# Performance work log

Hardware: AMD Instinct MI355X
Metric: run time of the kernel (lower is better)

Reference implementation:

```python
import jax, jax.numpy as jnp
import numpy as np

N = 96
M = 96
# visual field constants
L_V_EX, S_V_EX, L_V_IN, S_V_IN = 1.6, 3.5, 1.23, 6.3
FV, TAU_V, UPS_V, P_V, K_V = 1.0, 3.0, 3.0, 0.3, 7.0
# auditory field constants
L_A_EX, S_A_EX, L_A_IN, S_A_IN = 1.0, 5.3, 0.8, 11.8
FA, TAU_A, UPS_A, P_A, K_A = 1.0, 3.0, 3.0, 0.3, 3.0
# multisensory field constants
L_M_EX, S_M_EX, L_M_IN, S_M_IN = 3.8, 3.5, 3.3, 6.2
TAU_M, UPS_M, P_M = 3.0, 3.0, 0.3


def _torus_sqdist():
    # squared toroidal distance components: dx2[i,h], dy2[j,k]
    ii = jnp.arange(N, dtype=jnp.float32)
    jj = jnp.arange(M, dtype=jnp.float32)
    dx = jnp.abs(ii[:, None] - ii[None, :])
    dx = jnp.minimum(dx, N - dx)
    dy = jnp.abs(jj[:, None] - jj[None, :])
    dy = jnp.minimum(dy, M - dy)
    # aux[i,j,h,k] = dx[i,h]^2 + dy[j,k]^2
    return dx[:, None, :, None] ** 2 + dy[None, :, None, :] ** 2


def _dog(aux, l_ex, s_ex, l_in, s_in):
    # Faithful to source: exp(-aux/2 * sigma**2) == exp(-0.5*aux*sigma^2)
    return l_ex * jnp.exp(-0.5 * aux * (s_ex ** 2)) - l_in * jnp.exp(-0.5 * aux * (s_in ** 2))


def setup_inputs() -> dict:
    key = jax.random.key(0)
    ks = jax.random.split(key, 7)
    return {
        "video": jax.random.normal(ks[0], (32, 1024), dtype=jnp.float32),
        "audio": jax.random.normal(ks[1], (32, 2048), dtype=jnp.float32),
        "rf_v": jax.random.normal(ks[2], (N, M, 1024), dtype=jnp.float32) * (1.0 / np.sqrt(1024.0)),
        "rf_a": jax.random.normal(ks[3], (N, M, 2048), dtype=jnp.float32) * (1.0 / np.sqrt(2048.0)),
        "na_v": jax.random.normal(ks[4], (N, M), dtype=jnp.float32),
        "na_a": jax.random.normal(ks[5], (N, M), dtype=jnp.float32),
        "na_m": jax.random.normal(ks[6], (N, M), dtype=jnp.float32),
    }


def reference(video, audio, rf_v, rf_a, na_v, na_a, na_m):
    aux = _torus_sqdist()  # (N, M, N, M)
    syn_v = _dog(aux, L_V_EX, S_V_EX, L_V_IN, S_V_IN)
    syn_a = _dog(aux, L_A_EX, S_A_EX, L_A_IN, S_A_IN)
    syn_m = _dog(aux, L_M_EX, S_M_EX, L_M_IN, S_M_IN)

    # external inputs: sum over feature dim -> (B, N, M)
    ext_v = jnp.einsum('bv,ijv->bij', video, rf_v)
    ext_a = jnp.einsum('ba,ija->bij', audio, rf_a)

    # all-pairs neighbor inputs: neighbor[i,j] = sum_{h,k} act[h,k] * syn[i,j,h,k]
    nb_v = jnp.einsum('ijhk,hk->ij', syn_v, na_v)
    nb_a = jnp.einsum('ijhk,hk->ij', syn_a, na_a)

    coll_v = FV * na_m
    coll_a = FA * na_m

    na_v_new = na_v * (TAU_V - 1.0) / TAU_V + (1.0 / TAU_V) * jax.nn.sigmoid(
        (ext_v + nb_v - UPS_V + coll_v) * P_V)  # (B, N, M)
    na_a_new = na_a * (TAU_A - 1.0) / TAU_A + (1.0 / TAU_A) * jax.nn.sigmoid(
        (ext_a + nb_a - UPS_A + coll_a) * P_A)  # (B, N, M)

    nb_m = jnp.einsum('ijhk,hk->ij', syn_m, na_m)
    na_m_new = na_m * (TAU_M - 1.0) / TAU_M + (1.0 / TAU_M) * jax.nn.sigmoid(
        (K_V * na_v_new + K_A * na_a_new + nb_m - UPS_M) * P_M)  # (B, N, M)
    return na_m_new
```

## Files before the change

### kernel.cpp

```cpp
#include <hip/hip_runtime.h>
#include <math.h>

#define NN   96
#define NPOS (96*96)
#define BB   32
#define KV   1024
#define KA   2048
#define KCH  512
#define NCHV (KV/KCH)
#define NCHA (KA/KCH)
#define PT16 (NPOS/16)
#define NBLK_V (NCHV*PT16)
#define NBLK_A (NCHA*PT16)

#define PARTV_OFF 0
#define PARTA_OFF (NCHV*BB*NPOS)
#define CPT_OFF   (PARTA_OFF + NCHA*BB*NPOS)
#define AFV_OFF   (CPT_OFF + 6*NPOS)
#define AFV_SLOTS ((KV/32)*2*64)
#define AFA_OFF   (AFV_OFF + AFV_SLOTS*4)
#define AFA_SLOTS ((KA/32)*2*64)

typedef __bf16 bf16x8 __attribute__((ext_vector_type(8)));
typedef float  f32x4  __attribute__((ext_vector_type(4)));

__global__ __launch_bounds__(256) void nbT_kernel(
    const float* __restrict__ na_v, const float* __restrict__ na_a,
    const float* __restrict__ na_m, const float* __restrict__ video,
    const float* __restrict__ audio, float* __restrict__ ws)
{
    __shared__ float G[96][100];
    __shared__ float act_s[96][100];
    __shared__ float T1t[24][100];

    if (blockIdx.x >= 24) {
        const int e = (blockIdx.x - 24) * 256 + threadIdx.x;
        const float* src; bf16x8* dst; int K, el;
        if (e < AFV_SLOTS) { src = video; K = KV; dst = (bf16x8*)(ws + AFV_OFF); el = e; }
        else               { src = audio; K = KA; dst = (bf16x8*)(ws + AFA_OFF); el = e - AFV_SLOTS; }
        const int l  = el & 63;
        const int hb = (el >> 6) & 1;
        const int sg = el >> 7;
        const int b  = hb * 16 + (l & 15);
        const int k0 = sg * 32 + ((l >> 4) << 3);
        const float4 f0 = *(const float4*)&src[(size_t)b * K + k0];
        const float4 f1 = *(const float4*)&src[(size_t)b * K + k0 + 4];
        bf16x8 v;
        v[0] = (__bf16)f0.x; v[1] = (__bf16)f0.y; v[2] = (__bf16)f0.z; v[3] = (__bf16)f0.w;
        v[4] = (__bf16)f1.x; v[5] = (__bf16)f1.y; v[6] = (__bf16)f1.z; v[7] = (__bf16)f1.w;
        dst[el] = v;
        return;
    }

    const int c  = blockIdx.x >> 2;
    const int js = (blockIdx.x & 3) * 24;
    float l, s;
    if      (c == 0) { l =  1.60f; s = 3.5f;  }
    else if (c == 1) { l = -1.23f; s = 6.3f;  }
    else if (c == 2) { l =  1.00f; s = 5.3f;  }
    else if (c == 3) { l = -0.80f; s = 11.8f; }
    else if (c == 4) { l =  3.80f; s = 3.5f;  }
    else             { l = -3.30f; s = 6.2f;  }
    const float s2 = s * s;
    const int f = c >> 1;
    const float* act = (f == 0) ? na_v : (f == 1) ? na_a : na_m;
    const int tid = threadIdx.x;
    float* cpt = ws + CPT_OFF;

    for (int idx = tid; idx < 9216; idx += 256) {
        int j = idx / 96, k = idx - j * 96;
        int d = abs(j - k); d = min(d, 96 - d);
        G[j][k]     = __expf(-0.5f * (float)(d * d) * s2);
        act_s[j][k] = act[idx];
    }
    __syncthreads();

    const int hg3 = (tid >> 3) * 3;
    const int jl3 = (tid & 7) * 3;

    float t1[3][3] = {};
    for (int k0 = 0; k0 < 96; k0 += 4) {
        float4 av[3], gv[3];
        #pragma unroll
        for (int r = 0; r < 3; r++) {
            av[r] = *(const float4*)&act_s[hg3 + r][k0];
            gv[r] = *(const float4*)&G[js + jl3 + r][k0];
        }
        #pragma unroll
        for (int hh = 0; hh < 3; hh++)
            #pragma unroll
            for (int jj = 0; jj < 3; jj++)
                t1[hh][jj] += av[hh].x * gv[jj].x + av[hh].y * gv[jj].y
                            + av[hh].z * gv[jj].z + av[hh].w * gv[jj].w;
    }
    #pragma unroll
    for (int hh = 0; hh < 3; hh++)
        #pragma unroll
        for (int jj = 0; jj < 3; jj++)
            T1t[jl3 + jj][hg3 + hh] = t1[hh][jj];
    __syncthreads();

    float o[3][3] = {};
    for (int h0 = 0; h0 < 96; h0 += 4) {
        float4 gv[3], tv[3];
        #pragma unroll
        for (int r = 0; r < 3; r++) {
            gv[r] = *(const float4*)&G[hg3 + r][h0];
            tv[r] = *(const float4*)&T1t[jl3 + r][h0];
        }
        #pragma unroll
        for (int ii = 0; ii < 3; ii++)
            #pragma unroll
            for (int jj = 0; jj < 3; jj++)
                o[ii][jj] += gv[ii].x * tv[jj].x + gv[ii].y * tv[jj].y
                           + gv[ii].z * tv[jj].z + gv[ii].w * tv[jj].w;
    }
    #pragma unroll
    for (int ii = 0; ii < 3; ii++)
        #pragma unroll
        for (int jj = 0; jj < 3; jj++)
            cpt[c * NPOS + (hg3 + ii) * 96 + (js + jl3 + jj)] = l * o[ii][jj];
}

__global__ __launch_bounds__(64) void ext_mfma(
    const float* __restrict__ rf_v, const float* __restrict__ rf_a,
    float* __restrict__ ws)
{
    const int bid = blockIdx.x;
    const float* rf; const bf16x8* af; float* part; int K;
    int chunk, pt;
    if (bid < NBLK_V) {
        chunk = bid / PT16; pt = bid - chunk * PT16;
        rf = rf_v; K = KV;
        af = (const bf16x8*)(ws + AFV_OFF);
        part = ws + PARTV_OFF + (size_t)chunk * (BB * NPOS);
    } else {
        const int idx = bid - NBLK_V;
        chunk = idx / PT16; pt = idx - chunk * PT16;
        rf = rf_a; K = KA;
        af = (const bf16x8*)(ws + AFA_OFF);
        part = ws + PARTA_OFF + (size_t)chunk * (BB * NPOS);
    }
    const int kbase = chunk * KCH;
    const int l  = threadIdx.x;
    const int p0 = pt * 16;
    const int prow = p0 + (l & 15);
    const int koff = (l >> 4) * 8;
    const float4* bp = (const float4*)(rf + (size_t)prow * K + kbase + koff);
    const bf16x8* ap = af + (kbase >> 5) * 128 + l;

    f32x4 acc0 = {0.f, 0.f, 0.f, 0.f};
    f32x4 acc1 = {0.f, 0.f, 0.f, 0.f};

    #pragma unroll 4
    for (int st = 0; st < KCH / 32; ++st) {
        bf16x8 a0 = ap[st * 128];
        bf16x8 a1 = ap[st * 128 + 64];
        float4 f0 = bp[st * 8];
        float4 f1 = bp[st * 8 + 1];
        bf16x8 bv;
        bv[0] = (__bf16)f0.x; bv[1] = (__bf16)f0.y; bv[2] = (__bf16)f0.z; bv[3] = (__bf16)f0.w;
        bv[4] = (__bf16)f1.x; bv[5] = (__bf16)f1.y; bv[6] = (__bf16)f1.z; bv[7] = (__bf16)f1.w;
        acc0 = __builtin_amdgcn_mfma_f32_16x16x32_bf16(a0, bv, acc0, 0, 0, 0);
        acc1 = __builtin_amdgcn_mfma_f32_16x16x32_bf16(a1, bv, acc1, 0, 0, 0);
    }

    const int pcol  = p0 + (l & 15);
    const int brow0 = (l >> 4) * 4;
    #pragma unroll
    for (int r = 0; r < 4; ++r) {
        part[(size_t)(brow0 + r) * NPOS + pcol]        = acc0[r];
        part[(size_t)(16 + brow0 + r) * NPOS + pcol]   = acc1[r];
    }
}

__global__ __launch_bounds__(256) void combine_kernel(
    const float* __restrict__ na_v, const float* __restrict__ na_a,
    const float* __restrict__ na_m, const float* __restrict__ ws,
    float* __restrict__ out)
{
    const int npq = NPOS >> 2;
    const int t = blockIdx.x * 256 + threadIdx.x;
    if (t >= BB * npq) return;
    const int b  = t / npq;
    const int p0 = (t - b * npq) << 2;

    float4 ev = {0.f, 0.f, 0.f, 0.f}, ea = {0.f, 0.f, 0.f, 0.f};
    #pragma unroll
    for (int c = 0; c < NCHV; c++) {
        float4 x = *(const float4*)&ws[PARTV_OFF + (size_t)c * (BB * NPOS) + (size_t)b * NPOS + p0];
        ev.x += x.x; ev.y += x.y; ev.z += x.z; ev.w += x.w;
    }
    #pragma unroll
    for (int c = 0; c < NCHA; c++) {
        float4 x = *(const float4*)&ws[PARTA_OFF + (size_t)c * (BB * NPOS) + (size_t)b * NPOS + p0];
        ea.x += x.x; ea.y += x.y; ea.z += x.z; ea.w += x.w;
    }
    const float* cpt = ws + CPT_OFF;
    float4 q0 = *(const float4*)&cpt[0 * NPOS + p0];
    float4 q1 = *(const float4*)&cpt[1 * NPOS + p0];
    float4 q2 = *(const float4*)&cpt[2 * NPOS + p0];
    float4 q3 = *(const float4*)&cpt[3 * NPOS + p0];
    float4 q4 = *(const float4*)&cpt[4 * NPOS + p0];
    float4 q5 = *(const float4*)&cpt[5 * NPOS + p0];
    float4 nv = *(const float4*)&na_v[p0];
    float4 na = *(const float4*)&na_a[p0];
    float4 nm = *(const float4*)&na_m[p0];

    float evs[4] = {ev.x, ev.y, ev.z, ev.w};
    float eas[4] = {ea.x, ea.y, ea.z, ea.w};
    float nbv[4] = {q0.x + q1.x, q0.y + q1.y, q0.z + q1.z, q0.w + q1.w};
    float nba[4] = {q2.x + q3.x, q2.y + q3.y, q2.z + q3.z, q2.w + q3.w};
    float nbm[4] = {q4.x + q5.x, q4.y + q5.y, q4.z + q5.z, q4.w + q5.w};
    float nvs[4] = {nv.x, nv.y, nv.z, nv.w};
    float nas[4] = {na.x, na.y, na.z, na.w};
    float nms[4] = {nm.x, nm.y, nm.z, nm.w};

    float4 o;
    float* os = (float*)&o;
    #pragma unroll
    for (int u = 0; u < 4; u++) {
        const float xv = (evs[u] + nbv[u] - 3.0f + nms[u]) * 0.3f;
        const float nav_new = nvs[u] * (2.f / 3.f) + (1.f / 3.f) / (1.f + __expf(-xv));
        const float xa = (eas[u] + nba[u] - 3.0f + nms[u]) * 0.3f;
        const float naa_new = nas[u] * (2.f / 3.f) + (1.f / 3.f) / (1.f + __expf(-xa));
        const float xm = (7.0f * nav_new + 3.0f * naa_new + nbm[u] - 3.0f) * 0.3f;
        os[u] = nms[u] * (2.f / 3.f) + (1.f / 3.f) / (1.f + __expf(-xm));
    }
    *(float4*)&out[(size_t)b * NPOS + p0] = o;
}

extern "C" void kernel_launch(void* const* d_in, const int* in_sizes, int n_in,
                              void* d_out, int out_size, void* d_ws, size_t ws_size,
                              hipStream_t stream) {
    const float* video = (const float*)d_in[0];
    const float* audio = (const float*)d_in[1];
    const float* rf_v  = (const float*)d_in[2];
    const float* rf_a  = (const float*)d_in[3];
    const float* na_v  = (const float*)d_in[4];
    const float* na_a  = (const float*)d_in[5];
    const float* na_m  = (const float*)d_in[6];
    float* ws  = (float*)d_ws;
    float* out = (float*)d_out;

    nbT_kernel<<<72, 256, 0, stream>>>(na_v, na_a, na_m, video, audio, ws);
    ext_mfma<<<NBLK_V + NBLK_A, 64, 0, stream>>>(rf_v, rf_a, ws);
    combine_kernel<<<(BB * NPOS / 4 + 255) / 256, 256, 0, stream>>>(
        na_v, na_a, na_m, ws, out);
}
```

Before: 41.31 us.

## Pipeline ext GEMM through LDS with async global_load_lds and larger K chunks

Reworks the external-input MFMA kernel so each wave streams rf and activation tiles into a 4-deep LDS ring buffer via global_load_lds, using an XOR swizzle and explicit vmcnt waits. Global loads are overlapped with MFMA compute. The K chunk also grows from 512 to 1024, which cuts the partial-sum buffers (video is now one chunk, audio two) and shrinks the reduction in the combine kernel. The cost is fewer, longer blocks, which lowers parallelism, and a fragile pipeline built on hand-written inline asm.

```diff
diff --git a/kernel.cpp b/kernel.cpp
--- a/kernel.cpp
+++ b/kernel.cpp
@@ -6,16 +6,13 @@
 #define BB   32
 #define KV   1024
 #define KA   2048
-#define KCH  512
-#define NCHV (KV/KCH)
-#define NCHA (KA/KCH)
-#define PT16 (NPOS/16)
-#define NBLK_V (NCHV*PT16)
-#define NBLK_A (NCHA*PT16)
-
-#define PARTV_OFF 0
-#define PARTA_OFF (NCHV*BB*NPOS)
-#define CPT_OFF   (PARTA_OFF + NCHA*BB*NPOS)
+
+#define JOBS_A (2*576)
+
+#define EXTV_OFF  0
+#define EXTA0_OFF (BB*NPOS)
+#define EXTA1_OFF (2*BB*NPOS)
+#define CPT_OFF   (3*BB*NPOS)
 #define AFV_OFF   (CPT_OFF + 6*NPOS)
 #define AFV_SLOTS ((KV/32)*2*64)
 #define AFA_OFF   (AFV_OFF + AFV_SLOTS*4)
@@ -23,6 +20,9 @@
 
 typedef __bf16 bf16x8 __attribute__((ext_vector_type(8)));
 typedef float  f32x4  __attribute__((ext_vector_type(4)));
+typedef const __attribute__((address_space(1))) void* gas1_t;
+typedef __attribute__((address_space(3))) void*       las3_t;
+typedef const __attribute__((address_space(3))) char* lds3c_t;
 
 __global__ __launch_bounds__(256) void nbT_kernel(
     const float* __restrict__ na_v, const float* __restrict__ na_a,
@@ -126,51 +126,97 @@
     const float* __restrict__ rf_v, const float* __restrict__ rf_a,
     float* __restrict__ ws)
 {
+    __shared__ char lds[16384];
+    char* ldsc = (char*)lds;
     const int bid = blockIdx.x;
-    const float* rf; const bf16x8* af; float* part; int K;
-    int chunk, pt;
-    if (bid < NBLK_V) {
-        chunk = bid / PT16; pt = bid - chunk * PT16;
-        rf = rf_v; K = KV;
-        af = (const bf16x8*)(ws + AFV_OFF);
-        part = ws + PARTV_OFF + (size_t)chunk * (BB * NPOS);
+    const int l   = threadIdx.x;
+
+    const float* rf; const bf16x8* af; float* ext; int K, kb, pt;
+    if (bid < JOBS_A) {
+        const int c = bid / 576; pt = bid - c * 576;
+        rf = rf_a; K = KA; kb = c << 10;
+        af  = (const bf16x8*)(ws + AFA_OFF);
+        ext = ws + EXTA0_OFF + c * (BB * NPOS);
     } else {
-        const int idx = bid - NBLK_V;
-        chunk = idx / PT16; pt = idx - chunk * PT16;
-        rf = rf_a; K = KA;
-        af = (const bf16x8*)(ws + AFA_OFF);
-        part = ws + PARTA_OFF + (size_t)chunk * (BB * NPOS);
-    }
-    const int kbase = chunk * KCH;
-    const int l  = threadIdx.x;
-    const int p0 = pt * 16;
-    const int prow = p0 + (l & 15);
-    const int koff = (l >> 4) * 8;
-    const float4* bp = (const float4*)(rf + (size_t)prow * K + kbase + koff);
-    const bf16x8* ap = af + (kbase >> 5) * 128 + l;
+        pt = bid - JOBS_A; rf = rf_v; K = KV; kb = 0;
+        af  = (const bf16x8*)(ws + AFV_OFF);
+        ext = ws + EXTV_OFF;
+    }
+    const int p0 = pt << 4;
+
+    const int r8   = l >> 3;
+    const int csrc = (l & 7) ^ (r8 & 7);
+    const float*  rf0 = rf + (size_t)(p0 + r8) * K + kb + csrc * 4;
+    const float*  rf1 = rf0 + (size_t)8 * K;
+    const bf16x8* afA = af + (kb >> 5) * 128 + l;
+    const bf16x8* afB = afA + 64;
+
+    const int row   = l & 15, g = l >> 4;
+    const int roffA = row * 128 + ((((g << 1)    ) ^ (row & 7)) << 4);
+    const int roffB = row * 128 + ((((g << 1) | 1) ^ (row & 7)) << 4);
+    const int aoff  = l * 16;
+
+#define STAGE(tt, dd)                                                          \
+    do {                                                                       \
+        const int t_ = (tt);                                                   \
+        __builtin_amdgcn_global_load_lds((gas1_t)(rf0 + t_ * 32),              \
+            (las3_t)(ldsc + (dd) * 4096), 16, 0, 0);                           \
+        __builtin_amdgcn_global_load_lds((gas1_t)(rf1 + t_ * 32),              \
+            (las3_t)(ldsc + (dd) * 4096 + 1024), 16, 0, 0);                    \
+        __builtin_amdgcn_global_load_lds((gas1_t)(afA + t_ * 128),             \
+            (las3_t)(ldsc + (dd) * 4096 + 2048), 16, 0, 0);                    \
+        __builtin_amdgcn_global_load_lds((gas1_t)(afB + t_ * 128),             \
+            (las3_t)(ldsc + (dd) * 4096 + 3072), 16, 0, 0);                    \
+    } while (0)
+
+#define ITER(tt, dd, WAIT, DO_STAGE)                                           \
+    {                                                                          \
+        asm volatile("s_waitcnt vmcnt(" #WAIT ")");                            \
+        f32x4 rA, rB; bf16x8 av0, av1;                                         \
+        asm volatile("ds_read_b128 %0, %1" : "=v"(rA)                          \
+                     : "v"((lds3c_t)(ldsc + (dd) * 4096 + roffA)));            \
+        asm volatile("ds_read_b128 %0, %1" : "=v"(rB)                          \
+                     : "v"((lds3c_t)(ldsc + (dd) * 4096 + roffB)));            \
+        asm volatile("ds_read_b128 %0, %1" : "=v"(av0)                         \
+                     : "v"((lds3c_t)(ldsc + (dd) * 4096 + 2048 + aoff)));      \
+        asm volatile("ds_read_b128 %0, %1" : "=v"(av1)                         \
+                     : "v"((lds3c_t)(ldsc + (dd) * 4096 + 3072 + aoff)));      \
+        asm volatile("s_waitcnt lgkmcnt(0)");                                  \
+        __builtin_amdgcn_sched_barrier(0);                                     \
+        if (DO_STAGE) STAGE((tt) + 4, dd);                                     \
+        bf16x8 bv;                                                             \
+        bv[0] = (__bf16)rA[0]; bv[1] = (__bf16)rA[1];                          \
+        bv[2] = (__bf16)rA[2]; bv[3] = (__bf16)rA[3];                          \
+        bv[4] = (__bf16)rB[0]; bv[5] = (__bf16)rB[1];                          \
+        bv[6] = (__bf16)rB[2]; bv[7] = (__bf16)rB[3];                          \
+        acc0 = __builtin_amdgcn_mfma_f32_16x16x32_bf16(av0, bv, acc0, 0, 0, 0);\
+        acc1 = __builtin_amdgcn_mfma_f32_16x16x32_bf16(av1, bv, acc1, 0, 0, 0);\
+    }
 
     f32x4 acc0 = {0.f, 0.f, 0.f, 0.f};
     f32x4 acc1 = {0.f, 0.f, 0.f, 0.f};
 
-    #pragma unroll 4
-    for (int st = 0; st < KCH / 32; ++st) {
-        bf16x8 a0 = ap[st * 128];
-        bf16x8 a1 = ap[st * 128 + 64];
-        float4 f0 = bp[st * 8];
-        float4 f1 = bp[st * 8 + 1];
-        bf16x8 bv;
-        bv[0] = (__bf16)f0.x; bv[1] = (__bf16)f0.y; bv[2] = (__bf16)f0.z; bv[3] = (__bf16)f0.w;
-        bv[4] = (__bf16)f1.x; bv[5] = (__bf16)f1.y; bv[6] = (__bf16)f1.z; bv[7] = (__bf16)f1.w;
-        acc0 = __builtin_amdgcn_mfma_f32_16x16x32_bf16(a0, bv, acc0, 0, 0, 0);
-        acc1 = __builtin_amdgcn_mfma_f32_16x16x32_bf16(a1, bv, acc1, 0, 0, 0);
-    }
-
-    const int pcol  = p0 + (l & 15);
-    const int brow0 = (l >> 4) * 4;
+    STAGE(0, 0); STAGE(1, 1); STAGE(2, 2); STAGE(3, 3);
+
+    for (int t = 0; t < 28; t += 4) {
+        ITER(t + 0, 0, 12, 1);
+        ITER(t + 1, 1, 12, 1);
+        ITER(t + 2, 2, 12, 1);
+        ITER(t + 3, 3, 12, 1);
+    }
+    ITER(28, 0, 12, 0);
+    ITER(29, 1, 8,  0);
+    ITER(30, 2, 4,  0);
+    ITER(31, 3, 0,  0);
+#undef ITER
+#undef STAGE
+
+    const int pcol  = p0 + row;
+    const int brow0 = g * 4;
     #pragma unroll
     for (int r = 0; r < 4; ++r) {
-        part[(size_t)(brow0 + r) * NPOS + pcol]        = acc0[r];
-        part[(size_t)(16 + brow0 + r) * NPOS + pcol]   = acc1[r];
+        ext[(size_t)(brow0 + r) * NPOS + pcol]      = acc0[r];
+        ext[(size_t)(16 + brow0 + r) * NPOS + pcol] = acc1[r];
     }
 }
 
@@ -185,17 +231,10 @@
     const int b  = t / npq;
     const int p0 = (t - b * npq) << 2;
 
-    float4 ev = {0.f, 0.f, 0.f, 0.f}, ea = {0.f, 0.f, 0.f, 0.f};
-    #pragma unroll
-    for (int c = 0; c < NCHV; c++) {
-        float4 x = *(const float4*)&ws[PARTV_OFF + (size_t)c * (BB * NPOS) + (size_t)b * NPOS + p0];
-        ev.x += x.x; ev.y += x.y; ev.z += x.z; ev.w += x.w;
-    }
-    #pragma unroll
-    for (int c = 0; c < NCHA; c++) {
-        float4 x = *(const float4*)&ws[PARTA_OFF + (size_t)c * (BB * NPOS) + (size_t)b * NPOS + p0];
-        ea.x += x.x; ea.y += x.y; ea.z += x.z; ea.w += x.w;
-    }
+    float4 ev  = *(const float4*)&ws[EXTV_OFF  + (size_t)b * NPOS + p0];
+    float4 ea0 = *(const float4*)&ws[EXTA0_OFF + (size_t)b * NPOS + p0];
+    float4 ea1 = *(const float4*)&ws[EXTA1_OFF + (size_t)b * NPOS + p0];
+    float4 ea = {ea0.x + ea1.x, ea0.y + ea1.y, ea0.z + ea1.z, ea0.w + ea1.w};
     const float* cpt = ws + CPT_OFF;
     float4 q0 = *(const float4*)&cpt[0 * NPOS + p0];
     float4 q1 = *(const float4*)&cpt[1 * NPOS + p0];
@@ -244,7 +283,7 @@
     float* out = (float*)d_out;
 
     nbT_kernel<<<72, 256, 0, stream>>>(na_v, na_a, na_m, video, audio, ws);
-    ext_mfma<<<NBLK_V + NBLK_A, 64, 0, stream>>>(rf_v, rf_a, ws);
+    ext_mfma<<<JOBS_A + 576, 64, 0, stream>>>(rf_v, rf_a, ws);
     combine_kernel<<<(BB * NPOS / 4 + 255) / 256, 256, 0, stream>>>(
         na_v, na_a, na_m, ws, out);
 }
```

Result: faster. 40.10 us (-2.9%).
